# Kernel tuning notes

Measured on AMD Instinct MI355X. Metric: run time of the kernel, lower is better.

Reference implementation:

```python
import jax, jax.numpy as jnp
import numpy as np

N_HEAD = 16
D_MODEL = 1024
D_HEAD = 64
B = 2
S = 2048      # query length
M = 512       # memory length
K = S + M     # key length
L = 2 * K - 1 # relative position table length
SCALE = 1.0 / np.sqrt(D_MODEL)  # NOTE: module scales by 1/sqrt(d_model), not d_head
EPS = 1e-5


def layer_norm(x, gamma, beta):
    mu = jnp.mean(x, axis=-1, keepdims=True)
    var = jnp.mean(jnp.square(x - mu), axis=-1, keepdims=True)
    return (x - mu) * jax.lax.rsqrt(var + EPS) * gamma + beta


def skew(qpos, mem_len):
    # qpos: (B, H, S, 2K-1) -> relative-position scores aligned to keys (B, H, S, K)
    b, h, s, l = qpos.shape
    k_len = (l + 1) // 2
    pad = jnp.full((b, h, s, 1), -jnp.inf, dtype=qpos.dtype)
    rel = jnp.concatenate([qpos, pad], axis=-1)          # (B,H,S,2K)
    rel = rel.reshape(b, h, s * (l + 1))[..., : s * l]    # drop tail, shift rows
    rel = rel.reshape(b, h, s, l)
    start = (k_len - 1) - mem_len
    return rel[..., start : start + k_len]


def setup_inputs() -> dict:
    key = jax.random.key(0)
    ks = jax.random.split(key, 8)
    w_scale = 1.0 / np.sqrt(D_MODEL)
    hidden = jax.random.normal(ks[0], (B, S, D_MODEL), jnp.float32)
    memory = jax.random.normal(ks[1], (B, M, D_MODEL), jnp.float32)
    pos_emb = jax.random.normal(ks[2], (B, L, D_HEAD), jnp.float32)
    Wq = jax.random.normal(ks[3], (D_MODEL, N_HEAD * D_HEAD), jnp.float32) * w_scale
    Wk = jax.random.normal(ks[4], (D_MODEL, N_HEAD * D_HEAD), jnp.float32) * w_scale
    Wv = jax.random.normal(ks[5], (D_MODEL, N_HEAD * D_HEAD), jnp.float32) * w_scale
    Wo = jax.random.normal(ks[6], (N_HEAD * D_HEAD, D_MODEL), jnp.float32) * w_scale
    gamma = jnp.ones((D_MODEL,), jnp.float32)
    beta = jnp.zeros((D_MODEL,), jnp.float32)
    # causal mask with memory: query i may attend keys j <= i + M; True = drop
    i = jnp.arange(S)[:, None]
    j = jnp.arange(K)[None, :]
    mask = j > (i + M)  # (S, K) bool
    return {"hidden": hidden, "pos_emb": pos_emb, "memory": memory,
            "Wq": Wq, "Wk": Wk, "Wv": Wv, "Wo": Wo,
            "gamma": gamma, "beta": beta, "mask": mask}


def reference(hidden, pos_emb, memory, Wq, Wk, Wv, Wo, gamma, beta, mask):
    combined = jnp.concatenate([memory, hidden], axis=1)  # (B, K, D)
    hn = layer_norm(hidden, gamma, beta)                  # pre_lnorm
    cn = layer_norm(combined, gamma, beta)
    q = (hn @ Wq).reshape(B, S, N_HEAD, D_HEAD).transpose(0, 2, 1, 3)  # (B,H,S,Dh)
    k = (cn @ Wk).reshape(B, K, N_HEAD, D_HEAD).transpose(0, 2, 1, 3)  # (B,H,K,Dh)
    v = (cn @ Wv).reshape(B, K, N_HEAD, D_HEAD).transpose(0, 2, 1, 3)  # (B,H,K,Dh)
    scores = jnp.einsum("bhsd,bhkd->bhsk", q, k)           # content term
    qpos = jnp.einsum("bhsd,bld->bhsl", q, pos_emb)        # position term (B,H,S,2K-1)
    scores = (scores + skew(qpos, M)) * SCALE
    scores = jnp.where(mask[None, None], -jnp.inf, scores)
    attn = jax.nn.softmax(scores, axis=-1)
    atten_vec = jnp.einsum("bhsk,bhkd->bshd", attn, v).reshape(B, S, N_HEAD * D_HEAD)
    output = atten_vec @ Wo
    # faithful quirk: residual uses the layer-normed hidden when pre_lnorm=True
    return hn + output
```

## Files before the change

### kernel.cpp

```cpp
#include <hip/hip_runtime.h>

typedef unsigned short u16;
typedef float f32x4 __attribute__((ext_vector_type(4)));
typedef short short8 __attribute__((ext_vector_type(8)));

#define MFMA_BF16(a, b, c) __builtin_amdgcn_mfma_f32_16x16x32_bf16((a), (b), (c), 0, 0, 0)

#define NEG_BIG (-30000.0f)

typedef __attribute__((address_space(1))) const void gas_void;
typedef __attribute__((address_space(3))) void las_void;

__device__ __forceinline__ float bf2f(u16 v) {
  union { unsigned int u; float f; } c; c.u = ((unsigned int)v) << 16; return c.f;
}
__device__ __forceinline__ u16 f2bf(float f) {
  union { float f; unsigned int u; } c; c.f = f;
  return (u16)((c.u + 0x7fffu + ((c.u >> 16) & 1u)) >> 16);
}

__global__ __launch_bounds__(256) void cast_pe_k(const float* __restrict__ src, u16* __restrict__ dst, int n4) {
  const int idx = blockIdx.x * 256 + threadIdx.x;
  if (idx >= n4) return;
  const float4 d = *(const float4*)&src[idx * 4];
  ushort4 o;
  o.x = f2bf(d.x); o.y = f2bf(d.y); o.z = f2bf(d.z); o.w = f2bf(d.w);
  *(ushort4*)&dst[idx * 4] = o;
}

__global__ __launch_bounds__(256) void transpose_k(const float* __restrict__ W0, const float* __restrict__ W1,
                                                   const float* __restrict__ W2, const float* __restrict__ W3,
                                                   u16* __restrict__ Wt) {
  __shared__ float t[32][33];
  const float* W = (blockIdx.z == 0) ? W0 : (blockIdx.z == 1) ? W1 : (blockIdx.z == 2) ? W2 : W3;
  u16* dst = Wt + (size_t)blockIdx.z * 1024 * 1024;
  const int tx = threadIdx.x, ty = threadIdx.y;
  const int x0 = blockIdx.x * 32, y0 = blockIdx.y * 32;
#pragma unroll
  for (int i = 0; i < 32; i += 8)
    t[ty + i][tx] = W[(size_t)(y0 + ty + i) * 1024 + x0 + tx];
  __syncthreads();
#pragma unroll
  for (int i = 0; i < 32; i += 8)
    dst[(size_t)(x0 + ty + i) * 1024 + y0 + tx] = f2bf(t[tx][ty + i]);
}

__global__ __launch_bounds__(256) void ln_k(const float* __restrict__ hid, const float* __restrict__ mem,
                                            const float* __restrict__ gam, const float* __restrict__ bet,
                                            u16* __restrict__ cn) {
  const int row = blockIdx.x;
  const int b = (row >= 2560) ? 1 : 0;
  const int r = row - b * 2560;
  const float* src = (r < 512) ? (mem + ((size_t)b * 512 + r) * 1024)
                               : (hid + ((size_t)b * 2048 + (r - 512)) * 1024);
  const int tid = threadIdx.x;
  const float4 d = *(const float4*)&src[tid * 4];
  float x[4] = {d.x, d.y, d.z, d.w};
  float s = x[0] + x[1] + x[2] + x[3];
  float q = x[0]*x[0] + x[1]*x[1] + x[2]*x[2] + x[3]*x[3];
#pragma unroll
  for (int o = 1; o < 64; o <<= 1) { s += __shfl_xor(s, o); q += __shfl_xor(q, o); }
  __shared__ float sb[4], qsb[4];
  const int wave = tid >> 6;
  if ((tid & 63) == 0) { sb[wave] = s; qsb[wave] = q; }
  __syncthreads();
  s = sb[0] + sb[1] + sb[2] + sb[3];
  q = qsb[0] + qsb[1] + qsb[2] + qsb[3];
  const float mu = s * (1.0f / 1024.0f);
  const float var = q * (1.0f / 1024.0f) - mu * mu;
  const float rstd = rsqrtf(fmaxf(var, 0.0f) + 1e-5f);
  u16 o4[4];
#pragma unroll
  for (int i = 0; i < 4; ++i) {
    const int c = tid * 4 + i;
    o4[i] = f2bf((x[i] - mu) * rstd * gam[c] + bet[c]);
  }
  uint2 pk;
  pk.x = (unsigned)o4[0] | ((unsigned)o4[1] << 16);
  pk.y = (unsigned)o4[2] | ((unsigned)o4[3] << 16);
  *(uint2*)&cn[((size_t)b * 2560 + r) * 1024 + tid * 4] = pk;
}

__global__ __launch_bounds__(256, 3) void gemm128_k(const u16* __restrict__ A, const u16* __restrict__ Bt,
                                                    u16* __restrict__ qb, u16* __restrict__ kbo,
                                                    u16* __restrict__ vtb) {
  __shared__ u16 As[128][64];
  __shared__ u16 Bs[128][64];
  const int tid = threadIdx.x;
  const int lane = tid & 63, w = tid >> 6;
  const int quad = lane >> 4, l15 = lane & 15, r7 = l15 & 7;
  const int wr = w >> 1, wc = w & 1;
  const int row0 = blockIdx.y * 128, col0 = blockIdx.x * 128;
  const int rloc = w * 8 + (lane >> 3);
  const int cg = ((lane & 7) ^ ((lane >> 3) & 7)) * 8;
  const u16* ga = A + (size_t)(row0 + rloc) * 1024 + cg;
  const u16* gb = Bt + (size_t)(col0 + rloc) * 1024 + cg;
  f32x4 z = {0.f, 0.f, 0.f, 0.f};
  f32x4 acc[4][4];
#pragma unroll
  for (int m = 0; m < 4; ++m)
#pragma unroll
    for (int n = 0; n < 4; ++n) acc[m][n] = z;
  for (int kt = 0; kt < 16; ++kt) {
    const int k0 = kt * 64;
#pragma unroll
    for (int g2 = 0; g2 < 4; ++g2) {
      __builtin_amdgcn_global_load_lds((gas_void*)(ga + (size_t)g2 * 32 * 1024 + k0),
                                       (las_void*)(&As[g2 * 32 + w * 8][0]), 16, 0, 0);
      __builtin_amdgcn_global_load_lds((gas_void*)(gb + (size_t)g2 * 32 * 1024 + k0),
                                       (las_void*)(&Bs[g2 * 32 + w * 8][0]), 16, 0, 0);
    }
    __syncthreads();
    short8 af0[4], af1[4];
#pragma unroll
    for (int m = 0; m < 4; ++m) {
      const int row = wr * 64 + m * 16 + l15;
      af0[m] = *(const short8*)&As[row][(quad ^ r7) * 8];
      af1[m] = *(const short8*)&As[row][((quad + 4) ^ r7) * 8];
    }
#pragma unroll
    for (int n = 0; n < 4; ++n) {
      const int row = wc * 64 + n * 16 + l15;
      const short8 bf0 = *(const short8*)&Bs[row][(quad ^ r7) * 8];
      const short8 bf1 = *(const short8*)&Bs[row][((quad + 4) ^ r7) * 8];
#pragma unroll
      for (int m = 0; m < 4; ++m) {
        acc[m][n] = MFMA_BF16(af0[m], bf0, acc[m][n]);
        acc[m][n] = MFMA_BF16(af1[m], bf1, acc[m][n]);
      }
    }
    __syncthreads();
  }
  const int nc = col0 >> 10;
#pragma unroll
  for (int m = 0; m < 4; ++m) {
#pragma unroll
    for (int n = 0; n < 4; ++n) {
#pragma unroll
      for (int r = 0; r < 4; ++r) {
        const int R = row0 + wr * 64 + m * 16 + quad * 4 + r;
        const int C = col0 + wc * 64 + n * 16 + l15;
        const float v = acc[m][n][r];
        const int c = C & 1023, h = c >> 6, dh = c & 63;
        const int b = (R >= 2560) ? 1 : 0, kk = R - b * 2560;
        if (nc == 0) {
          if (kk >= 512)
            qb[(((size_t)(b * 16 + h)) * 2048 + (kk - 512)) * 64 + dh] = f2bf(v * 0.03125f);
        } else if (nc == 1) {
          kbo[(((size_t)(b * 16 + h)) * 2560 + kk) * 64 + dh] = f2bf(v);
        } else {
          vtb[(((size_t)(b * 16 + h)) * 64 + dh) * 2560 + kk] = f2bf(v);
        }
      }
    }
  }
}

__global__ __launch_bounds__(256) void gemm_out_k(const u16* __restrict__ A, const u16* __restrict__ Bt,
                                                  float* __restrict__ outf,
                                                  const u16* __restrict__ resid) {
  __shared__ u16 As[2][64][40];
  __shared__ u16 Bs[2][64][40];
  const int tid = threadIdx.x;
  const int lane = tid & 63, wave = tid >> 6;
  const int quad = lane >> 4, l15 = lane & 15;
  const int row0 = blockIdx.y * 64, col0 = blockIdx.x * 64;
  const int sr = tid >> 2, sc8 = (tid & 3) * 8;
  const u16* ga = A + (size_t)(row0 + sr) * 1024 + sc8;
  const u16* gb = Bt + (size_t)(col0 + sr) * 1024 + sc8;
  f32x4 z = {0.f, 0.f, 0.f, 0.f};
  f32x4 acc[4];
#pragma unroll
  for (int i = 0; i < 4; ++i) acc[i] = z;
  *(uint4*)&As[0][sr][sc8] = *(const uint4*)ga;
  *(uint4*)&Bs[0][sr][sc8] = *(const uint4*)gb;
  __syncthreads();
  for (int it = 0; it < 32; ++it) {
    const int cur = it & 1;
    const int kn = (it + 1 < 32) ? (it + 1) * 32 : it * 32;
    const uint4 ua = *(const uint4*)(ga + kn);
    const uint4 ub = *(const uint4*)(gb + kn);
    const short8 af = *(const short8*)&As[cur][16 * wave + l15][quad * 8];
#pragma unroll
    for (int n = 0; n < 4; ++n)
      acc[n] = MFMA_BF16(af, *(const short8*)&Bs[cur][16 * n + l15][quad * 8], acc[n]);
    *(uint4*)&As[cur ^ 1][sr][sc8] = ua;
    *(uint4*)&Bs[cur ^ 1][sr][sc8] = ub;
    __syncthreads();
  }
#pragma unroll
  for (int n = 0; n < 4; ++n) {
#pragma unroll
    for (int r = 0; r < 4; ++r) {
      const int R = row0 + 16 * wave + quad * 4 + r;
      const int C = col0 + 16 * n + l15;
      const size_t rrow = (size_t)(R >> 11) * 2560 + 512 + (R & 2047);
      outf[(size_t)R * 1024 + C] = acc[n][r] + bf2f(resid[rrow * 1024 + C]);
    }
  }
}

__global__ __launch_bounds__(512, 4) void attn_k(const u16* __restrict__ q, const u16* __restrict__ kb,
                                                 const u16* __restrict__ vt, const u16* __restrict__ pe,
                                                 u16* __restrict__ av) {
  __shared__ u16 Kt[2][64][72];
  __shared__ u16 Vt[2][64][72];
  __shared__ u16 Pw[8][16][68];
  const int tid = threadIdx.x, lane = tid & 63, wave = tid >> 6;
  const int quad = lane >> 4, l15 = lane & 15;
  const int bh = blockIdx.y, b = bh >> 4, h = bh & 15;
  const int qt = (blockIdx.y < 16) ? (15 - blockIdx.x) : blockIdx.x;
  const int i0 = qt * 128;
  const int qi0 = i0 + wave * 16;
  const u16* qrow = q + ((size_t)bh * 2048 + qi0 + l15) * 64 + quad * 8;
  const short8 aq0 = *(const short8*)qrow;
  const short8 aq1 = *(const short8*)(qrow + 32);
  const u16* pp = pe + ((long)b * 5119 - qi0 + 2032 + l15) * 64 + quad * 8;
  const int sr = tid >> 3, sc8 = (tid & 7) * 8;
  f32x4 z = {0.f, 0.f, 0.f, 0.f};
  f32x4 acc[4];
#pragma unroll
  for (int i = 0; i < 4; ++i) acc[i] = z;
  float lrow[4] = {0.f, 0.f, 0.f, 0.f};
  const int ntiles = 2 * qt + 10;
  const int jlast = qi0 + 527;
  *(uint4*)&Kt[0][sr][sc8] = *(const uint4*)&kb[((size_t)bh * 2560 + sr) * 64 + sc8];
  *(uint4*)&Vt[0][sr][sc8] = *(const uint4*)&vt[((size_t)bh * 64 + sr) * 2560 + sc8];
  __syncthreads();
  for (int jt = 0; jt < ntiles; ++jt) {
    const int j0 = jt * 64;
    const int cur = jt & 1;
    const int jn = (jt + 1 < ntiles) ? (jt + 1) : jt;
    const uint4 ku = *(const uint4*)&kb[((size_t)bh * 2560 + jn * 64 + sr) * 64 + sc8];
    const uint4 vu = *(const uint4*)&vt[((size_t)bh * 64 + sr) * 2560 + jn * 64 + sc8];
    if (j0 <= jlast) {
      short8 pb[5], pb2[5];
#pragma unroll
      for (int g = 0; g < 5; ++g) {
        pb[g]  = *(const short8*)(pp + 1024 * g);
        pb2[g] = *(const short8*)(pp + 1024 * g + 32);
      }
      f32x4 sc[4];
#pragma unroll
      for (int s = 0; s < 4; ++s) {
        sc[s] = MFMA_BF16(aq0, *(const short8*)&Kt[cur][16 * s + l15][quad * 8], z);
        sc[s] = MFMA_BF16(aq1, *(const short8*)&Kt[cur][16 * s + l15][32 + quad * 8], sc[s]);
      }
      f32x4 qp[5];
#pragma unroll
      for (int g = 0; g < 5; ++g) {
        qp[g] = MFMA_BF16(aq0, pb[g], z);
        qp[g] = MFMA_BF16(aq1, pb2[g], qp[g]);
      }
#pragma unroll
      for (int r = 0; r < 4; ++r) {
        const int di = quad * 4 + r;
        const int o = l15 - di + 15;
        const int src = quad * 16 + (o & 15);
        const float g0 = __shfl(qp[0][r], src);
        const float g1 = __shfl(qp[1][r], src);
        const float g2 = __shfl(qp[2][r], src);
        const float g3 = __shfl(qp[3][r], src);
        const float g4 = __shfl(qp[4][r], src);
        const bool lo = (o < 16);
        float s0 = sc[0][r] + (lo ? g0 : g1);
        float s1 = sc[1][r] + (lo ? g1 : g2);
        float s2 = sc[2][r] + (lo ? g2 : g3);
        float s3 = sc[3][r] + (lo ? g3 : g4);
        const int jlim = qi0 + di + 512 - j0 - l15;
        if (0 > jlim)  s0 = NEG_BIG;
        if (16 > jlim) s1 = NEG_BIG;
        if (32 > jlim) s2 = NEG_BIG;
        if (48 > jlim) s3 = NEG_BIG;
        const float p0 = __expf(s0);
        const float p1 = __expf(s1);
        const float p2 = __expf(s2);
        const float p3 = __expf(s3);
        lrow[r] += (p0 + p1) + (p2 + p3);
        Pw[wave][di][l15]      = f2bf(p0);
        Pw[wave][di][16 + l15] = f2bf(p1);
        Pw[wave][di][32 + l15] = f2bf(p2);
        Pw[wave][di][48 + l15] = f2bf(p3);
      }
      asm volatile("s_waitcnt lgkmcnt(0)" ::: "memory");
      const short8 pf0 = *(const short8*)&Pw[wave][l15][quad * 8];
      const short8 pf1 = *(const short8*)&Pw[wave][l15][32 + quad * 8];
#pragma unroll
      for (int n = 0; n < 4; ++n) {
        acc[n] = MFMA_BF16(pf0, *(const short8*)&Vt[cur][16 * n + l15][quad * 8], acc[n]);
        acc[n] = MFMA_BF16(pf1, *(const short8*)&Vt[cur][16 * n + l15][32 + quad * 8], acc[n]);
      }
    }
    *(uint4*)&Kt[cur ^ 1][sr][sc8] = ku;
    *(uint4*)&Vt[cur ^ 1][sr][sc8] = vu;
    __syncthreads();
    pp += 4096;
  }
#pragma unroll
  for (int r = 0; r < 4; ++r) {
    float lsum = lrow[r];
#pragma unroll
    for (int o = 1; o < 16; o <<= 1) lsum += __shfl_xor(lsum, o);
    const float inv = 1.0f / lsum;
    const int s = qi0 + quad * 4 + r;
#pragma unroll
    for (int n = 0; n < 4; ++n) {
      const int c = h * 64 + n * 16 + l15;
      av[((size_t)b * 2048 + s) * 1024 + c] = f2bf(acc[n][r] * inv);
    }
  }
}

extern "C" void kernel_launch(void* const* d_in, const int* in_sizes, int n_in,
                              void* d_out, int out_size, void* d_ws, size_t ws_size,
                              hipStream_t stream) {
  const float* hidden = (const float*)d_in[0];
  const float* pe     = (const float*)d_in[1];
  const float* memv   = (const float*)d_in[2];
  const float* Wq     = (const float*)d_in[3];
  const float* Wk     = (const float*)d_in[4];
  const float* Wv     = (const float*)d_in[5];
  const float* Wo     = (const float*)d_in[6];
  const float* gam    = (const float*)d_in[7];
  const float* bet    = (const float*)d_in[8];

  u16* ws  = (u16*)d_ws;
  u16* cn  = ws;
  u16* qb  = cn  + (size_t)5120 * 1024;
  u16* kb  = qb  + (size_t)4096 * 1024;
  u16* vt  = kb  + (size_t)5120 * 1024;
  u16* av  = vt  + (size_t)5120 * 1024;
  u16* wt  = av  + (size_t)4096 * 1024;
  u16* peb = wt  + (size_t)4 * 1024 * 1024;

  const int pe_n4 = (2 * 5119 * 64) / 4;
  cast_pe_k<<<(pe_n4 + 255) / 256, 256, 0, stream>>>(pe, peb, pe_n4);
  ln_k<<<5120, 256, 0, stream>>>(hidden, memv, gam, bet, cn);
  transpose_k<<<dim3(32, 32, 4), dim3(32, 8), 0, stream>>>(Wq, Wk, Wv, Wo, wt);
  gemm128_k<<<dim3(24, 40), 256, 0, stream>>>(cn, wt, qb, kb, vt);
  attn_k<<<dim3(16, 32), 512, 0, stream>>>(qb, kb, vt, peb, av);
  gemm_out_k<<<dim3(16, 64), 256, 0, stream>>>(av, wt + (size_t)3 * 1024 * 1024,
                                               (float*)d_out, cn);
}
```

Baseline: 357.4 us.

## Split attention key range across two blocks and combine partial results

Each query tile's key loop is split into two halves handled by separate blocks, which doubles the grid from 512 to 1024 blocks. Each half writes unnormalized bf16 partial outputs and row sums, and a new combine kernel adds them and normalizes. The aim is better occupancy and load balance across the GPU's compute units for the causal attention. The cost is an extra kernel launch, extra global traffic for partial outputs, and rounding the unnormalized partials to bf16. The combine is plain addition because the kernel uses no running max, so this relies on scores staying small enough for exp without overflow.

```diff
diff --git a/kernel.cpp b/kernel.cpp
--- a/kernel.cpp
+++ b/kernel.cpp
@@ -202,35 +202,38 @@
 
 __global__ __launch_bounds__(512, 4) void attn_k(const u16* __restrict__ q, const u16* __restrict__ kb,
                                                  const u16* __restrict__ vt, const u16* __restrict__ pe,
-                                                 u16* __restrict__ av) {
+                                                 u16* __restrict__ p0, u16* __restrict__ p1,
+                                                 float* __restrict__ l0, float* __restrict__ l1) {
   __shared__ u16 Kt[2][64][72];
   __shared__ u16 Vt[2][64][72];
   __shared__ u16 Pw[8][16][68];
   const int tid = threadIdx.x, lane = tid & 63, wave = tid >> 6;
   const int quad = lane >> 4, l15 = lane & 15;
   const int bh = blockIdx.y, b = bh >> 4, h = bh & 15;
-  const int qt = (blockIdx.y < 16) ? (15 - blockIdx.x) : blockIdx.x;
+  const int qt = (blockIdx.y < 16) ? (15 - (blockIdx.x >> 1)) : (blockIdx.x >> 1);
+  const int half = blockIdx.x & 1;
   const int i0 = qt * 128;
   const int qi0 = i0 + wave * 16;
   const u16* qrow = q + ((size_t)bh * 2048 + qi0 + l15) * 64 + quad * 8;
   const short8 aq0 = *(const short8*)qrow;
   const short8 aq1 = *(const short8*)(qrow + 32);
-  const u16* pp = pe + ((long)b * 5119 - qi0 + 2032 + l15) * 64 + quad * 8;
+  const int nh = qt + 5;
+  const int t0 = half * nh, t1 = t0 + nh;
+  const u16* pp = pe + ((long)b * 5119 - qi0 + 2032 + l15) * 64 + quad * 8 + (size_t)t0 * 4096;
   const int sr = tid >> 3, sc8 = (tid & 7) * 8;
   f32x4 z = {0.f, 0.f, 0.f, 0.f};
   f32x4 acc[4];
 #pragma unroll
   for (int i = 0; i < 4; ++i) acc[i] = z;
   float lrow[4] = {0.f, 0.f, 0.f, 0.f};
-  const int ntiles = 2 * qt + 10;
   const int jlast = qi0 + 527;
-  *(uint4*)&Kt[0][sr][sc8] = *(const uint4*)&kb[((size_t)bh * 2560 + sr) * 64 + sc8];
-  *(uint4*)&Vt[0][sr][sc8] = *(const uint4*)&vt[((size_t)bh * 64 + sr) * 2560 + sc8];
+  *(uint4*)&Kt[0][sr][sc8] = *(const uint4*)&kb[((size_t)bh * 2560 + t0 * 64 + sr) * 64 + sc8];
+  *(uint4*)&Vt[0][sr][sc8] = *(const uint4*)&vt[((size_t)bh * 64 + sr) * 2560 + t0 * 64 + sc8];
   __syncthreads();
-  for (int jt = 0; jt < ntiles; ++jt) {
+  for (int jt = t0; jt < t1; ++jt) {
     const int j0 = jt * 64;
-    const int cur = jt & 1;
-    const int jn = (jt + 1 < ntiles) ? (jt + 1) : jt;
+    const int cur = (jt - t0) & 1;
+    const int jn = (jt + 1 < t1) ? (jt + 1) : jt;
     const uint4 ku = *(const uint4*)&kb[((size_t)bh * 2560 + jn * 64 + sr) * 64 + sc8];
     const uint4 vu = *(const uint4*)&vt[((size_t)bh * 64 + sr) * 2560 + jn * 64 + sc8];
     if (j0 <= jlast) {
@@ -272,15 +275,15 @@
         if (16 > jlim) s1 = NEG_BIG;
         if (32 > jlim) s2 = NEG_BIG;
         if (48 > jlim) s3 = NEG_BIG;
-        const float p0 = __expf(s0);
-        const float p1 = __expf(s1);
-        const float p2 = __expf(s2);
-        const float p3 = __expf(s3);
-        lrow[r] += (p0 + p1) + (p2 + p3);
-        Pw[wave][di][l15]      = f2bf(p0);
-        Pw[wave][di][16 + l15] = f2bf(p1);
-        Pw[wave][di][32 + l15] = f2bf(p2);
-        Pw[wave][di][48 + l15] = f2bf(p3);
+        const float p0v = __expf(s0);
+        const float p1v = __expf(s1);
+        const float p2v = __expf(s2);
+        const float p3v = __expf(s3);
+        lrow[r] += (p0v + p1v) + (p2v + p3v);
+        Pw[wave][di][l15]      = f2bf(p0v);
+        Pw[wave][di][16 + l15] = f2bf(p1v);
+        Pw[wave][di][32 + l15] = f2bf(p2v);
+        Pw[wave][di][48 + l15] = f2bf(p3v);
       }
       asm volatile("s_waitcnt lgkmcnt(0)" ::: "memory");
       const short8 pf0 = *(const short8*)&Pw[wave][l15][quad * 8];
@@ -296,19 +299,41 @@
     __syncthreads();
     pp += 4096;
   }
+  u16* od = half ? p1 : p0;
+  float* ol = half ? l1 : l0;
 #pragma unroll
   for (int r = 0; r < 4; ++r) {
     float lsum = lrow[r];
 #pragma unroll
     for (int o = 1; o < 16; o <<= 1) lsum += __shfl_xor(lsum, o);
-    const float inv = 1.0f / lsum;
     const int s = qi0 + quad * 4 + r;
+    if (l15 == 0) ol[(size_t)bh * 2048 + s] = lsum;
 #pragma unroll
     for (int n = 0; n < 4; ++n) {
       const int c = h * 64 + n * 16 + l15;
-      av[((size_t)b * 2048 + s) * 1024 + c] = f2bf(acc[n][r] * inv);
-    }
-  }
+      od[((size_t)b * 2048 + s) * 1024 + c] = f2bf(acc[n][r]);
+    }
+  }
+}
+
+__global__ __launch_bounds__(256) void combine_k(u16* __restrict__ av, const u16* __restrict__ p1,
+                                                 const float* __restrict__ l0, const float* __restrict__ l1) {
+  const int idx = blockIdx.x * 256 + threadIdx.x;
+  const int base = idx * 4;
+  const int row = base >> 10;
+  const int col = base & 1023;
+  const int b = row >> 11, s = row & 2047;
+  const int h = col >> 6;
+  const size_t li = ((size_t)(b * 16 + h)) * 2048 + s;
+  const float inv = 1.0f / (l0[li] + l1[li]);
+  const ushort4 a0 = *(const ushort4*)&av[(size_t)base];
+  const ushort4 a1 = *(const ushort4*)&p1[(size_t)base];
+  ushort4 o;
+  o.x = f2bf((bf2f(a0.x) + bf2f(a1.x)) * inv);
+  o.y = f2bf((bf2f(a0.y) + bf2f(a1.y)) * inv);
+  o.z = f2bf((bf2f(a0.z) + bf2f(a1.z)) * inv);
+  o.w = f2bf((bf2f(a0.w) + bf2f(a1.w)) * inv);
+  *(ushort4*)&av[(size_t)base] = o;
 }
 
 extern "C" void kernel_launch(void* const* d_in, const int* in_sizes, int n_in,
@@ -332,13 +357,17 @@
   u16* av  = vt  + (size_t)5120 * 1024;
   u16* wt  = av  + (size_t)4096 * 1024;
   u16* peb = wt  + (size_t)4 * 1024 * 1024;
+  u16* p1  = peb + (size_t)2 * 5119 * 64;
+  float* l0 = (float*)(p1 + (size_t)4096 * 1024);
+  float* l1 = l0 + (size_t)32 * 2048;
 
   const int pe_n4 = (2 * 5119 * 64) / 4;
   cast_pe_k<<<(pe_n4 + 255) / 256, 256, 0, stream>>>(pe, peb, pe_n4);
   ln_k<<<5120, 256, 0, stream>>>(hidden, memv, gam, bet, cn);
   transpose_k<<<dim3(32, 32, 4), dim3(32, 8), 0, stream>>>(Wq, Wk, Wv, Wo, wt);
   gemm128_k<<<dim3(24, 40), 256, 0, stream>>>(cn, wt, qb, kb, vt);
-  attn_k<<<dim3(16, 32), 512, 0, stream>>>(qb, kb, vt, peb, av);
+  attn_k<<<dim3(32, 32), 512, 0, stream>>>(qb, kb, vt, peb, av, p1, l0, l1);
+  combine_k<<<4096, 256, 0, stream>>>(av, p1, l0, l1);
   gemm_out_k<<<dim3(16, 64), 256, 0, stream>>>(av, wt + (size_t)3 * 1024 * 1024,
                                                (float*)d_out, cn);
 }
```

After: 419.1 us. 17.3% more time.
